# Performance work log

Measured on AMD Instinct MI355X. Metric: run time of the kernel, lower is better.

## Reference

```python
import jax, jax.numpy as jnp
import numpy as np

B, T, C, H, N = 2, 1024, 2048, 32, 64
KVH = 8                       # GQA kv heads
KV = KVH * N                  # 512
REP = H // KVH                # 4
EPS = 1e-6
LORA = [96, 96, 64, 256, 64]  # xw, xa, xv, xg, xk lora dims


def rmsnorm(x, w, eps=EPS):
    xf = x.astype(jnp.float32)
    var = jnp.mean(xf * xf, axis=-1, keepdims=True)
    return (w * (xf * jax.lax.rsqrt(var + eps))).astype(x.dtype)


def rotate_half(x):
    x1, x2 = jnp.split(x, 2, axis=-1)
    return jnp.concatenate([-x2, x1], axis=-1)


def rwkv7_scan(r, w, k, v, a, b, state0):
    # r,w,k,v,a,b: [B,T,H,N]; state0: [B,H,N,N] (value x key)
    # per step: S = S*exp(w) + (S@a) b^T + v k^T ; o = S @ r
    def step(S, inp):
        r_t, w_t, k_t, v_t, a_t, b_t = inp  # each [B,H,N]
        sa = jnp.einsum('bhvk,bhk->bhv', S, a_t)
        S = (S * jnp.exp(w_t)[:, :, None, :]
             + sa[..., None] * b_t[:, :, None, :]
             + v_t[..., None] * k_t[:, :, None, :])
        o = jnp.einsum('bhvk,bhk->bhv', S, r_t)
        return S, o
    seqs = tuple(jnp.moveaxis(t, 1, 0) for t in (r, w, k, v, a, b))
    S, o = jax.lax.scan(step, state0, seqs)
    return jnp.moveaxis(o, 0, 1), S


def setup_inputs() -> dict:
    key = jax.random.key(0)
    ks = jax.random.split(key, 24)
    g = lambda i, shape, s=0.02: jax.random.normal(ks[i], shape, jnp.float32) * s
    # real rope cache, theta = 1e6, rotary_dim = N
    pos = jnp.arange(T, dtype=jnp.float32)
    inv = 1.0 / (1e6 ** (jnp.arange(0, N, 2, dtype=jnp.float32) / N))
    ang = pos[:, None] * inv[None, :]
    ang = jnp.concatenate([ang, ang], axis=-1)  # [T, N]
    cos = jnp.broadcast_to(jnp.cos(ang)[None], (B, T, N))
    sin = jnp.broadcast_to(jnp.sin(ang)[None], (B, T, N))
    return dict(
        x_in=jax.random.normal(ks[0], (B, T, C), jnp.float32),
        v_first=jax.random.normal(ks[1], (B, T, KVH, N), jnp.float32),
        k_first=jax.random.normal(ks[2], (B, T, KVH, N), jnp.float32),
        state=jnp.zeros((B, H, N, N), jnp.float32),
        calc_cos=cos, calc_sin=sin,
        ln1=jnp.ones((C,), jnp.float32), ln2=jnp.ones((C,), jnp.float32),
        ln_r=jnp.ones((N,), jnp.float32), ln_k=jnp.ones((N,), jnp.float32),
        wavgk1=g(3, (C, sum(LORA))),
        w0=g(4, (H * N,)), w2=g(5, (LORA[0], H * N)),
        a0=g(6, (H * N,)), a2=g(7, (LORA[1], H * N)),
        v0=g(8, (KV,)), v2=g(9, (LORA[2], KV)),
        k0=g(10, (KV,)), k2=g(11, (LORA[4], KV)),
        g2=g(12, (LORA[3], H * N)),
        r_k=g(13, (H, N)),
        RKV_W=g(14, (C, H * N + 2 * KV)),
        O_W=g(15, (H * N, C)),
        R_bias=g(16, (H * N,)), K_bias=g(17, (KV,)), V_bias=g(18, (KV,)),
    )


def _forward(x_in, v_first, k_first, state, calc_cos, calc_sin,
             ln1, ln2, ln_r, ln_k, wavgk1, w0, w2, a0, a2, v0, v2,
             k0, k2, g2, r_k, RKV_W, O_W, R_bias, K_bias, V_bias):
    x = rmsnorm(x_in, ln1)
    xw, xa, xv, xg, xk = jnp.split(x @ wavgk1, np.cumsum(LORA)[:-1].tolist(), axis=-1)
    r, k, v = jnp.split(x @ RKV_W, [H * N, H * N + KV], axis=-1)
    r = (r + R_bias).reshape(B, T, H, N)
    k = (k + K_bias).reshape(B, T, KVH, N)
    v = (v + V_bias).reshape(B, T, KVH, N)
    r = rmsnorm(r, ln_r)
    k = rmsnorm(k, ln_k)
    cos = calc_cos[:, :, None, :]
    sin = calc_sin[:, :, None, :]
    r = r * cos + rotate_half(r) * sin
    k = k * cos + rotate_half(k) * sin
    # layer_id != 0: sigmoid-gated interpolation toward first-layer v/k
    v = v + (v_first - v) * jax.nn.sigmoid(xv @ v2 + v0).reshape(B, T, KVH, N)
    k = k + (k_first - k) * jax.nn.sigmoid(xk @ k2 + k0).reshape(B, T, KVH, N)
    # GQA repeat (contiguous per kv head, as repeat_kv does)
    k = jnp.repeat(k, REP, axis=2).reshape(B, T, H * N)
    v = jnp.repeat(v, REP, axis=2).reshape(B, T, H * N)
    a = jax.nn.sigmoid(xa @ a2 + a0)
    kh = k.reshape(B, T, H, N)
    kk = (kh / (jnp.linalg.norm(kh, axis=-1, keepdims=True) + 1e-12)).reshape(B, T, H * N)
    w = jnp.tanh(xw) @ w2 + w0
    w = -jax.nn.softplus(-w) - 0.5
    k = k * (1.0 - w + a)
    aa = -kk
    bb = kk * a
    wlog = -jnp.exp(w)
    sh = (B, T, H, N)
    o, state = rwkv7_scan(r, wlog.reshape(sh), k.reshape(sh), v.reshape(sh),
                          aa.reshape(sh), bb.reshape(sh), state)
    xx = o.reshape(B, T, H * N) * (float(N) ** -0.5)
    bonus = ((r * k.reshape(sh) * r_k).sum(axis=-1, keepdims=True)
             * v.reshape(sh)).reshape(B, T, H * N)
    xx = xx + bonus
    out = (xx * (jax.nn.sigmoid(xg) @ g2)) @ O_W
    x_res = x_in + out
    output = rmsnorm(x_res, ln2)
    return output, x[:, -1], state, v_first, k_first, x_res


def reference(x_in, v_first, k_first, state, calc_cos, calc_sin,
              ln1, ln2, ln_r, ln_k, wavgk1, w0, w2, a0, a2, v0, v2,
              k0, k2, g2, r_k, RKV_W, O_W, R_bias, K_bias, V_bias):
    return _forward(x_in, v_first, k_first, state, calc_cos, calc_sin,
                    ln1, ln2, ln_r, ln_k, wavgk1, w0, w2, a0, a2, v0, v2,
                    k0, k2, g2, r_k, RKV_W, O_W, R_bias, K_bias, V_bias)
```

## Files before the change

kernel.cpp:

```cpp
#include <hip/hip_runtime.h>
#include <hip/hip_bf16.h>

#define BT 2
#define TT 1024
#define CC 2048
#define HH 32
#define MM (BT*TT)
#define TCH 512
#define NCH (TT/TCH)
#define RECB 896

typedef __attribute__((ext_vector_type(8))) short short8;
typedef __attribute__((ext_vector_type(4))) float floatx4;
typedef __attribute__((ext_vector_type(2))) float f32x2;

static __device__ __forceinline__ float bf2f(__hip_bfloat16 x){ return __bfloat162float(x); }
static __device__ __forceinline__ __hip_bfloat16 f2bf(float x){ return __float2bfloat16(x); }
static __device__ __forceinline__ float sigm(float x){ return 1.0f/(1.0f + expf(-x)); }
static __device__ __forceinline__ float u2f(unsigned short u){
  union { unsigned int i; float f; } x; x.i = ((unsigned int)u) << 16; return x.f;
}
static __device__ __forceinline__ float ulo(unsigned int u){ return __uint_as_float(u << 16); }
static __device__ __forceinline__ float uhi(unsigned int u){ return __uint_as_float(u & 0xffff0000u); }
static __device__ __forceinline__ unsigned short bfbits(float x){
  __hip_bfloat16 h = f2bf(x);
  unsigned short s; __builtin_memcpy(&s, &h, 2); return s;
}
static __device__ __forceinline__ unsigned int pkbf(float lo, float hi){
  return (unsigned int)bfbits(lo) | ((unsigned int)bfbits(hi) << 16);
}

#if defined(__has_builtin)
#if __has_builtin(__builtin_amdgcn_global_load_lds)
#define HAVE_GLL 1
#endif
#endif

#ifdef HAVE_GLL
static __device__ __forceinline__ void gll16(const void* g, void* l){
  __builtin_amdgcn_global_load_lds(
      (__attribute__((address_space(1))) void*)const_cast<void*>(g),
      (__attribute__((address_space(3))) void*)l,
      16, 0, 0);
}
#endif

#define DPP_ADD(x, ctrl) ((x) + __int_as_float(__builtin_amdgcn_update_dpp(0, __float_as_int(x), (ctrl), 0xF, 0xF, true)))

#if defined(__has_builtin)
#if __has_builtin(__builtin_amdgcn_permlane16_swap) && __has_builtin(__builtin_amdgcn_permlane32_swap)
#define HAVE_PLSWAP 1
#endif
#endif

#ifdef HAVE_PLSWAP
typedef unsigned int uint2v __attribute__((ext_vector_type(2)));
static __device__ __forceinline__ float row16_pair_add(float x){
  unsigned int u = __float_as_uint(x);
  uint2v r = __builtin_amdgcn_permlane16_swap(u, u, false, false);
  return __uint_as_float(r[0]) + __uint_as_float(r[1]);
}
static __device__ __forceinline__ float half32_pair_add(float x){
  unsigned int u = __float_as_uint(x);
  uint2v r = __builtin_amdgcn_permlane32_swap(u, u, false, false);
  return __uint_as_float(r[0]) + __uint_as_float(r[1]);
}
#else
static __device__ __forceinline__ float row16_pair_add(float x){ return x + __shfl_xor(x, 16); }
static __device__ __forceinline__ float half32_pair_add(float x){ return x + __shfl_xor(x, 32); }
#endif

static __device__ __forceinline__ float red8(float x){
  x = DPP_ADD(x, 0xB1);
  x = DPP_ADD(x, 0x4E);
  x = DPP_ADD(x, 0x141);
  return x;
}
static __device__ __forceinline__ float red32(float x){
  x = DPP_ADD(x, 0xB1);
  x = DPP_ADD(x, 0x4E);
  x = DPP_ADD(x, 0x124);
  x = DPP_ADD(x, 0x128);
  return row16_pair_add(x);
}
static __device__ __forceinline__ float red64(float x){
  x = DPP_ADD(x, 0xB1);
  x = DPP_ADD(x, 0x4E);
  x = DPP_ADD(x, 0x124);
  x = DPP_ADD(x, 0x128);
  x = row16_pair_add(x);
  return half32_pair_add(x);
}

__global__ __launch_bounds__(256) void tcvt_kernel(
    const float* __restrict__ W, __hip_bfloat16* __restrict__ Wt,
    int K, int N, int Npad)
{
  __shared__ float tile[32][33];
  const int bn = blockIdx.x*32, bk = blockIdx.y*32;
  const int tx = threadIdx.x & 31, ty0 = threadIdx.x >> 5;
#pragma unroll
  for (int i=0;i<4;++i){
    const int kk = bk + ty0 + i*8;
    float val = 0.f;
    if (kk < K && bn + tx < N) val = W[(size_t)kk*N + bn + tx];
    tile[ty0 + i*8][tx] = val;
  }
  __syncthreads();
#pragma unroll
  for (int i=0;i<4;++i){
    const int nn = bn + ty0 + i*8;
    const int kk = bk + tx;
    if (nn < Npad && kk < K) Wt[(size_t)nn*K + kk] = f2bf(tile[tx][ty0 + i*8]);
  }
}

__global__ __launch_bounds__(256) void rmsnorm1_kernel(
    const float* __restrict__ x_in,
    const float* __restrict__ ln1,
    __hip_bfloat16* __restrict__ x_bf,
    float* __restrict__ x_last)
{
  const int m = blockIdx.x;
  const int tid = threadIdx.x;
  const int c = tid * 8;
  const float* xp = x_in + (size_t)m*CC + c;
  float v[8]; float ss = 0.f;
#pragma unroll
  for (int i=0;i<8;++i){ v[i] = xp[i]; ss += v[i]*v[i]; }
  ss = red64(ss);
  __shared__ float wsum[4];
  if ((tid&63)==0) wsum[tid>>6] = ss;
  __syncthreads();
  ss = wsum[0]+wsum[1]+wsum[2]+wsum[3];
  const float sc = rsqrtf(ss * (1.0f/CC) + 1e-6f);
#pragma unroll
  for (int i=0;i<8;++i) {
    const float y = ln1[c+i] * v[i] * sc;
    x_bf[(size_t)m*CC + c + i] = f2bf(y);
    if ((m % TT) == TT-1) x_last[(size_t)(m/TT)*CC + c + i] = y;
  }
}

template<bool F32OUT, int ACT>
__global__ __launch_bounds__(256) void mgemm(
    const __hip_bfloat16* __restrict__ A, int lda,
    const __hip_bfloat16* __restrict__ Bt,
    void* __restrict__ C, int N, int K)
{
  __shared__ __align__(16) short As[128*32];
  __shared__ __align__(16) short Bs[128*32];
  const int tid = threadIdx.x;
  const int bm = blockIdx.x * 128;
  const int bn = blockIdx.y * 128;
  const int wid = tid >> 6;
  const int lane = tid & 63;
  const int m16 = lane & 15, quad = lane >> 4;
  const int wm = wid & 1, wn = wid >> 1;
  const int lrow = tid >> 2;
  const int lcol = (tid & 3) * 8;

  floatx4 acc[4][4];
#pragma unroll
  for (int i=0;i<4;++i)
#pragma unroll
    for (int j=0;j<4;++j) acc[i][j] = (floatx4){0.f,0.f,0.f,0.f};

  char* asl = (char*)As + tid*16;
  char* bsl = (char*)Bs + tid*16;

  for (int k0 = 0; k0 < K; k0 += 32) {
    __syncthreads();
#ifdef HAVE_GLL
    gll16(A  + (size_t)(bm + lrow)      * lda + k0 + lcol, asl);
    gll16(A  + (size_t)(bm + 64 + lrow) * lda + k0 + lcol, asl + 4096);
    gll16(Bt + (size_t)(bn + lrow)      * K   + k0 + lcol, bsl);
    gll16(Bt + (size_t)(bn + 64 + lrow) * K   + k0 + lcol, bsl + 4096);
#else
    uint4 a0v = *(const uint4*)(const void*)(A  + (size_t)(bm + lrow)      * lda + k0 + lcol);
    uint4 a1v = *(const uint4*)(const void*)(A  + (size_t)(bm + 64 + lrow) * lda + k0 + lcol);
    uint4 b0v = *(const uint4*)(const void*)(Bt + (size_t)(bn + lrow)      * K   + k0 + lcol);
    uint4 b1v = *(const uint4*)(const void*)(Bt + (size_t)(bn + 64 + lrow) * K   + k0 + lcol);
    *(uint4*)(void*)(asl)        = a0v;
    *(uint4*)(void*)(asl + 4096) = a1v;
    *(uint4*)(void*)(bsl)        = b0v;
    *(uint4*)(void*)(bsl + 4096) = b1v;
#endif
    __syncthreads();

    short8 af[4], bfg[4];
#pragma unroll
    for (int mi=0; mi<4; ++mi)
      af[mi] = *(const short8*)(const void*)(As + (wm*64 + mi*16 + m16)*32 + quad*8);
#pragma unroll
    for (int ni=0; ni<4; ++ni)
      bfg[ni] = *(const short8*)(const void*)(Bs + (wn*64 + ni*16 + m16)*32 + quad*8);
#pragma unroll
    for (int mi=0; mi<4; ++mi)
#pragma unroll
      for (int ni=0; ni<4; ++ni)
        acc[mi][ni] = __builtin_amdgcn_mfma_f32_16x16x32_bf16(af[mi], bfg[ni], acc[mi][ni], 0,0,0);
  }

#pragma unroll
  for (int mi=0; mi<4; ++mi) {
    const int row = bm + wm*64 + mi*16 + quad*4;
#pragma unroll
    for (int ni=0; ni<4; ++ni) {
      const int col = bn + wn*64 + ni*16 + m16;
      if (col < N) {
        if (F32OUT) {
          float* cp = (float*)C;
#pragma unroll
          for (int r=0;r<4;++r) cp[(size_t)(row+r)*N + col] = acc[mi][ni][r];
        } else {
          __hip_bfloat16* cp = (__hip_bfloat16*)C;
#pragma unroll
          for (int r=0;r<4;++r) {
            float x = acc[mi][ni][r];
            if (ACT == 1) {
              if (col < 96) x = tanhf(x);
              else if (col >= 256 && col < 512) x = sigm(x);
            }
            cp[(size_t)(row+r)*N + col] = f2bf(x);
          }
        }
      }
    }
  }
}

__global__ __launch_bounds__(256) void prep_kernel(
    const __hip_bfloat16* __restrict__ RKV,
    const __hip_bfloat16* __restrict__ Wpre,
    const __hip_bfloat16* __restrict__ Apre,
    const __hip_bfloat16* __restrict__ Vsig,
    const __hip_bfloat16* __restrict__ Ksig,
    const float* __restrict__ v_first,
    const float* __restrict__ k_first,
    const float* __restrict__ cosp,
    const float* __restrict__ sinp,
    const float* __restrict__ ln_r,
    const float* __restrict__ ln_k,
    const float* __restrict__ r_k,
    const float* __restrict__ w0,
    const float* __restrict__ a0,
    const float* __restrict__ v0,
    const float* __restrict__ k0b,
    const float* __restrict__ R_bias,
    const float* __restrict__ K_bias,
    const float* __restrict__ V_bias,
    char* __restrict__ rec,
    float* __restrict__ bonus,
    int t0)
{
  const int b    = blockIdx.x / TCH;
  const int tloc = blockIdx.x % TCH;
  const int t    = t0 + tloc;
  const int m    = b*TT + t;
  const int tid = threadIdx.x;
  const int h  = tid >> 3;
  const int j  = tid & 7;
  const int hk = h >> 2;
  const int nb = j * 8;
  const int hn = h*64 + nb;
  const int kn = hk*64 + nb;

  const size_t rbase = (size_t)m*3072 + h*64 + nb;
  const size_t kbase = (size_t)m*3072 + 2048 + kn;
  const size_t vbase = kbase + 512;

  float r[8], k[8], v[8];
  float ssr = 0.f, ssk = 0.f;
#pragma unroll
  for (int i=0;i<8;++i) {
    r[i] = bf2f(RKV[rbase+i]) + R_bias[hn+i];
    k[i] = bf2f(RKV[kbase+i]) + K_bias[kn+i];
    v[i] = bf2f(RKV[vbase+i]) + V_bias[kn+i];
    ssr += r[i]*r[i];
    ssk += k[i]*k[i];
  }
  ssr = red8(ssr);
  ssk = red8(ssk);
  const float scr = rsqrtf(ssr*(1.0f/64.0f) + 1e-6f);
  const float sck = rsqrtf(ssk*(1.0f/64.0f) + 1e-6f);
#pragma unroll
  for (int i=0;i<8;++i) {
    r[i] = ln_r[nb+i] * r[i] * scr;
    k[i] = ln_k[nb+i] * k[i] * sck;
  }
  const float sgn = (j < 4) ? -1.0f : 1.0f;
  float rr[8], kr[8];
#pragma unroll
  for (int i=0;i<8;++i) {
    const float cs = cosp[(size_t)m*64 + nb + i];
    const float sn = sinp[(size_t)m*64 + nb + i];
    const float pr = __shfl_xor(r[i], 4);
    const float pk = __shfl_xor(k[i], 4);
    rr[i] = r[i]*cs + sgn*pr*sn;
    kr[i] = k[i]*cs + sgn*pk*sn;
  }
  float av[8], ew[8], wv2[8];
  float ssn = 0.f;
#pragma unroll
  for (int i=0;i<8;++i) {
    const float vs = sigm(bf2f(Vsig[(size_t)m*512 + kn + i]) + v0[kn+i]);
    v[i]  = v[i]  + (v_first[(size_t)m*512 + kn + i] - v[i])  * vs;
    const float ks = sigm(bf2f(Ksig[(size_t)m*512 + kn + i]) + k0b[kn+i]);
    kr[i] = kr[i] + (k_first[(size_t)m*512 + kn + i] - kr[i]) * ks;
    ssn += kr[i]*kr[i];
    av[i] = sigm(bf2f(Apre[(size_t)m*2048 + hn + i]) + a0[hn+i]);
    float wraw = bf2f(Wpre[(size_t)m*2048 + hn + i]) + w0[hn+i];
    const float xs = -wraw;
    const float sp = fmaxf(xs, 0.f) + log1pf(expf(-fabsf(xs)));
    const float wv = -sp - 0.5f;
    wv2[i] = wv;
    ew[i] = expf(-expf(wv));
  }
  ssn = red8(ssn);
  const float inrm = 1.0f / (sqrtf(ssn) + 1e-12f);
  float kf[8], kkv[8];
  float bsum = 0.f;
#pragma unroll
  for (int i=0;i<8;++i) {
    kkv[i] = kr[i] * inrm;
    kf[i]  = kr[i] * (1.0f - wv2[i] + av[i]);
    bsum  += rr[i] * kf[i] * r_k[hn+i];
  }
  bsum = red8(bsum);

  char* base = rec + ((size_t)(b*HH + h)*TCH + tloc)*RECB;
  const int klb = nb >> 1;
#pragma unroll
  for (int p=0;p<4;++p) {
    const int i0 = 2*p, i1 = i0 + 1;
    uint4 Aw;
    Aw.x = __float_as_uint(ew[i0]);
    Aw.y = __float_as_uint(ew[i1]);
    Aw.z = pkbf(rr[i0], rr[i1]);
    Aw.w = pkbf(kf[i0], kf[i1]);
    *(uint4*)(void*)(base + (size_t)(klb + p)*16) = Aw;
    uint2 Bw;
    Bw.x = pkbf(kkv[i0], kkv[i1]);
    Bw.y = pkbf(-kkv[i0]*av[i0], -kkv[i1]*av[i1]);
    *(uint2*)(void*)(base + 512 + (size_t)(klb + p)*8) = Bw;
  }
  short8 vs8;
#pragma unroll
  for (int i=0;i<8;++i) vs8[i] = (short)bfbits(v[i]);
  *(short8*)(void*)(base + 768 + (size_t)nb*2) = vs8;
#pragma unroll
  for (int i=0;i<8;++i)
    bonus[(size_t)m*2048 + hn + i] = bsum * v[i];
}

__global__ __launch_bounds__(256) void scan_kernel(
    const char* __restrict__ rec,
    float* __restrict__ state,
    float* __restrict__ o_out,
    int t0)
{
  const int blk = blockIdx.x;
  const int bh  = blk & 63;
  const int q   = blk >> 6;
  const int b   = bh >> 5, h = bh & 31;
  const int tid = threadIdx.x;
  const int vl  = q*8 + (tid >> 5);
  const int kl  = tid & 31;
  const int k2  = kl*2;

  const char* base = rec + (size_t)bh * TCH * RECB;
  float* sp = state + ((size_t)bh*64 + vl)*64 + k2;
  f32x2 S; S.x = sp[0]; S.y = sp[1];

  const char* pA = base + kl*16;
  const char* pB = base + 512 + kl*8;
  const char* pv = base + 768 + vl*2;

  uint4 Ab[4]; uint2 Bb[4]; unsigned short vb[4];
#pragma unroll
  for (int s=0;s<4;++s){
    Ab[s] = *(const uint4*)(const void*)(pA + s*RECB);
    Bb[s] = *(const uint2*)(const void*)(pB + s*RECB);
    vb[s] = *(const unsigned short*)(const void*)(pv + s*RECB);
  }
  pA += 4*RECB; pB += 4*RECB; pv += 4*RECB;

  int oidx = (b*TT + t0)*CC + h*64 + vl - CC;
  float opart = 0.f;

#define SCAN_STEP(jj, PF, ST)                                                  \
  {                                                                            \
    const uint4 A  = Ab[jj];                                                   \
    const uint2 Bv = Bb[jj];                                                   \
    const float vf = u2f(vb[jj]);                                              \
    if (PF) {                                                                  \
      Ab[jj] = *(const uint4*)(const void*)(pA + jj*RECB);                     \
      Bb[jj] = *(const uint2*)(const void*)(pB + jj*RECB);                     \
      vb[jj] = *(const unsigned short*)(const void*)(pv + jj*RECB);            \
    }                                                                          \
    float op = red32(opart);                                                   \
    f32x2 kk; kk.x = ulo(Bv.x); kk.y = uhi(Bv.x);                              \
    const f32x2 prod = S * kk;                                                 \
    float sa = prod.x + prod.y;                                                \
    sa = red32(sa);                                                            \
    if (ST && kl == 0) o_out[oidx] = op;                                       \
    f32x2 ew; ew.x = __uint_as_float(A.x); ew.y = __uint_as_float(A.y);        \
    f32x2 bb; bb.x = ulo(Bv.y); bb.y = uhi(Bv.y);                              \
    f32x2 kf; kf.x = ulo(A.w); kf.y = uhi(A.w);                                \
    f32x2 sav; sav.x = sa; sav.y = sa;                                         \
    f32x2 vfv; vfv.x = vf; vfv.y = vf;                                         \
    S = S*ew + sav*bb + vfv*kf;                                                \
    f32x2 rv; rv.x = ulo(A.z); rv.y = uhi(A.z);                                \
    const f32x2 ov = S * rv;                                                   \
    opart = ov.x + ov.y;                                                       \
    oidx += CC;                                                                \
  }

  SCAN_STEP(0, true, 0)
  SCAN_STEP(1, true, 1)
  SCAN_STEP(2, true, 1)
  SCAN_STEP(3, true, 1)
  pA += 4*RECB; pB += 4*RECB; pv += 4*RECB;

  for (int t = 4; t < TCH-4; t += 4) {
    SCAN_STEP(0, true, 1)
    SCAN_STEP(1, true, 1)
    SCAN_STEP(2, true, 1)
    SCAN_STEP(3, true, 1)
    pA += 4*RECB; pB += 4*RECB; pv += 4*RECB;
  }
  SCAN_STEP(0, false, 1)
  SCAN_STEP(1, false, 1)
  SCAN_STEP(2, false, 1)
  SCAN_STEP(3, false, 1)
#undef SCAN_STEP

  opart = red32(opart);
  if (kl == 0)
    o_out[oidx] = opart;

  sp[0]=S.x; sp[1]=S.y;
}

__global__ void xxg_kernel(const float* __restrict__ o_in,
                           const float* __restrict__ bonus,
                           const __hip_bfloat16* __restrict__ G,
                           __hip_bfloat16* __restrict__ xxg)
{
  int i = blockIdx.x*256 + threadIdx.x;
  xxg[i] = f2bf((o_in[i]*0.125f + bonus[i]) * bf2f(G[i]));
}

__global__ __launch_bounds__(256) void final_kernel(
    const float* __restrict__ x_in,
    const float* __restrict__ OUTb,
    const float* __restrict__ ln2,
    float* __restrict__ seg0,
    float* __restrict__ seg5)
{
  const int m = blockIdx.x;
  const int tid = threadIdx.x;
  const int c = tid*8;
  const float* xp = x_in + (size_t)m*CC + c;
  const float* op = OUTb + (size_t)m*CC + c;
  float xr[8]; float ss = 0.f;
#pragma unroll
  for (int i=0;i<8;++i){ xr[i] = xp[i] + op[i]; ss += xr[i]*xr[i]; }
#pragma unroll
  for (int i=0;i<8;++i) seg5[(size_t)m*CC + c + i] = xr[i];
  ss = red64(ss);
  __shared__ float wsum[4];
  if ((tid&63)==0) wsum[tid>>6] = ss;
  __syncthreads();
  ss = wsum[0]+wsum[1]+wsum[2]+wsum[3];
  const float sc = rsqrtf(ss*(1.0f/CC) + 1e-6f);
#pragma unroll
  for (int i=0;i<8;++i) seg0[(size_t)m*CC + c + i] = ln2[c+i] * xr[i] * sc;
}

extern "C" void kernel_launch(void* const* d_in, const int* in_sizes, int n_in,
                              void* d_out, int out_size, void* d_ws, size_t ws_size,
                              hipStream_t stream)
{
  (void)in_sizes; (void)n_in; (void)out_size; (void)ws_size;
  const float* x_in   = (const float*)d_in[0];
  const float* v_first= (const float*)d_in[1];
  const float* k_first= (const float*)d_in[2];
  const float* state0 = (const float*)d_in[3];
  const float* cosp   = (const float*)d_in[4];
  const float* sinp   = (const float*)d_in[5];
  const float* ln1    = (const float*)d_in[6];
  const float* ln2    = (const float*)d_in[7];
  const float* ln_r   = (const float*)d_in[8];
  const float* ln_k   = (const float*)d_in[9];
  const float* wavgk1 = (const float*)d_in[10];
  const float* w0     = (const float*)d_in[11];
  const float* w2     = (const float*)d_in[12];
  const float* a0     = (const float*)d_in[13];
  const float* a2     = (const float*)d_in[14];
  const float* v0     = (const float*)d_in[15];
  const float* v2     = (const float*)d_in[16];
  const float* k0b    = (const float*)d_in[17];
  const float* k2     = (const float*)d_in[18];
  const float* g2     = (const float*)d_in[19];
  const float* r_k    = (const float*)d_in[20];
  const float* RKV_W  = (const float*)d_in[21];
  const float* O_W    = (const float*)d_in[22];
  const float* R_bias = (const float*)d_in[23];
  const float* K_bias = (const float*)d_in[24];
  const float* V_bias = (const float*)d_in[25];

  float* out  = (float*)d_out;
  float* seg0 = out;
  float* seg1 = out + 4194304;
  float* seg2 = out + 4198400;
  float* seg3 = out + 4460544;
  float* seg4 = out + 5509120;
  float* seg5 = out + 6557696;

  char* ws = (char*)d_ws;
  const size_t OFF_STF   = 0;
  const size_t OFF_OWT   = 1048576;
  const size_t OFF_G     = 9437184;
  const size_t OFF_VSIG  = 17825792;
  const size_t OFF_KSIG  = 19922944;
  const size_t OFF_WPRE  = 22020096;
  const size_t OFF_APRE  = 30408704;
  const size_t OFF_RKV   = 38797312;
  const size_t OFF_XBF   = 51380224;
  const size_t OFF_Y1    = 59768832;
  const size_t OFF_WT    = 62128128;
  const size_t OFF_WAVT  = OFF_WT;
  const size_t OFF_RKVT  = OFF_WAVT + 2621440;
  const size_t OFF_W2T   = OFF_RKVT + 12582912;
  const size_t OFF_A2T   = OFF_W2T  + 393216;
  const size_t OFF_V2T   = OFF_A2T  + 393216;
  const size_t OFF_K2T   = OFF_V2T  + 65536;
  const size_t OFF_G2T   = OFF_K2T  + 65536;
  const size_t OFF_REC   = OFF_WT;
  const size_t OFF_XXG   = OFF_XBF;
  const size_t OFF_OUT   = OFF_WPRE;

  float*          stf   = (float*)(ws + OFF_STF);
  __hip_bfloat16* owt   = (__hip_bfloat16*)(ws + OFF_OWT);
  __hip_bfloat16* Gbuf  = (__hip_bfloat16*)(ws + OFF_G);
  __hip_bfloat16* Vsig  = (__hip_bfloat16*)(ws + OFF_VSIG);
  __hip_bfloat16* Ksig  = (__hip_bfloat16*)(ws + OFF_KSIG);
  __hip_bfloat16* Wpre  = (__hip_bfloat16*)(ws + OFF_WPRE);
  __hip_bfloat16* Apre  = (__hip_bfloat16*)(ws + OFF_APRE);
  __hip_bfloat16* RKV   = (__hip_bfloat16*)(ws + OFF_RKV);
  __hip_bfloat16* x_bf  = (__hip_bfloat16*)(ws + OFF_XBF);
  __hip_bfloat16* Y1    = (__hip_bfloat16*)(ws + OFF_Y1);
  __hip_bfloat16* wavt  = (__hip_bfloat16*)(ws + OFF_WAVT);
  __hip_bfloat16* rkvt  = (__hip_bfloat16*)(ws + OFF_RKVT);
  __hip_bfloat16* w2t   = (__hip_bfloat16*)(ws + OFF_W2T);
  __hip_bfloat16* a2t   = (__hip_bfloat16*)(ws + OFF_A2T);
  __hip_bfloat16* v2t   = (__hip_bfloat16*)(ws + OFF_V2T);
  __hip_bfloat16* k2t   = (__hip_bfloat16*)(ws + OFF_K2T);
  __hip_bfloat16* g2t   = (__hip_bfloat16*)(ws + OFF_G2T);
  char*           rec   = ws + OFF_REC;
  __hip_bfloat16* xxg   = (__hip_bfloat16*)(ws + OFF_XXG);
  float*          OUTb  = (float*)(ws + OFF_OUT);

  float* o_st = seg0;
  float* b_st = seg5;

  tcvt_kernel<<<dim3(20, 64), 256, 0, stream>>>(wavgk1, wavt, 2048, 576, 640);
  tcvt_kernel<<<dim3(96, 64), 256, 0, stream>>>(RKV_W,  rkvt, 2048, 3072, 3072);
  tcvt_kernel<<<dim3(64, 64), 256, 0, stream>>>(O_W,    owt,  2048, 2048, 2048);
  tcvt_kernel<<<dim3(64,  3), 256, 0, stream>>>(w2,     w2t,    96, 2048, 2048);
  tcvt_kernel<<<dim3(64,  3), 256, 0, stream>>>(a2,     a2t,    96, 2048, 2048);
  tcvt_kernel<<<dim3(16,  2), 256, 0, stream>>>(v2,     v2t,    64,  512,  512);
  tcvt_kernel<<<dim3(16,  2), 256, 0, stream>>>(k2,     k2t,    64,  512,  512);
  tcvt_kernel<<<dim3(64,  8), 256, 0, stream>>>(g2,     g2t,   256, 2048, 2048);

  rmsnorm1_kernel<<<MM, 256, 0, stream>>>(x_in, ln1, x_bf, seg1);
  mgemm<false,1><<<dim3(16,  5), 256, 0, stream>>>(x_bf, CC, wavt, Y1,   576, 2048);
  mgemm<false,0><<<dim3(16, 24), 256, 0, stream>>>(x_bf, CC, rkvt, RKV, 3072, 2048);
  mgemm<false,0><<<dim3(16, 16), 256, 0, stream>>>(Y1+0,   576, w2t, Wpre, 2048, 96);
  mgemm<false,0><<<dim3(16, 16), 256, 0, stream>>>(Y1+96,  576, a2t, Apre, 2048, 96);
  mgemm<false,0><<<dim3(16,  4), 256, 0, stream>>>(Y1+192, 576, v2t, Vsig,  512, 64);
  mgemm<false,0><<<dim3(16,  4), 256, 0, stream>>>(Y1+512, 576, k2t, Ksig,  512, 64);
  mgemm<false,0><<<dim3(16, 16), 256, 0, stream>>>(Y1+256, 576, g2t, Gbuf, 2048, 256);

  hipMemcpyAsync(stf, state0, (size_t)1048576, hipMemcpyDeviceToDevice, stream);
  for (int c = 0; c < NCH; ++c) {
    const int t0 = c*TCH;
    prep_kernel<<<BT*TCH, 256, 0, stream>>>(RKV, Wpre, Apre, Vsig, Ksig, v_first, k_first,
                                            cosp, sinp, ln_r, ln_k, r_k, w0, a0, v0, k0b,
                                            R_bias, K_bias, V_bias, rec, b_st, t0);
    scan_kernel<<<BT*HH*8, 256, 0, stream>>>(rec, stf, o_st, t0);
  }
  hipMemcpyAsync(seg2, stf, (size_t)1048576, hipMemcpyDeviceToDevice, stream);

  xxg_kernel<<<(MM*CC)/256, 256, 0, stream>>>(o_st, b_st, Gbuf, xxg);
  mgemm<true,0><<<dim3(16, 16), 256, 0, stream>>>(xxg, CC, owt, OUTb, 2048, 2048);
  final_kernel<<<MM, 256, 0, stream>>>(x_in, OUTb, ln2, seg0, seg5);

  hipMemcpyAsync(seg3, v_first, (size_t)1048576*4, hipMemcpyDeviceToDevice, stream);
  hipMemcpyAsync(seg4, k_first, (size_t)1048576*4, hipMemcpyDeviceToDevice, stream);
}
```

Baseline: 664.8 us.

## Merge LoRA up-projections into one block-diagonal GEMM and pair scan steps

```diff
diff --git a/kernel.cpp b/kernel.cpp
--- a/kernel.cpp
+++ b/kernel.cpp
@@ -8,11 +8,11 @@
 #define MM (BT*TT)
 #define TCH 512
 #define NCH (TT/TCH)
+#define YS 7168
 #define RECB 896
 
 typedef __attribute__((ext_vector_type(8))) short short8;
 typedef __attribute__((ext_vector_type(4))) float floatx4;
-typedef __attribute__((ext_vector_type(2))) float f32x2;
 
 static __device__ __forceinline__ float bf2f(__hip_bfloat16 x){ return __bfloat162float(x); }
 static __device__ __forceinline__ __hip_bfloat16 f2bf(float x){ return __float2bfloat16(x); }
@@ -94,7 +94,7 @@
 
 __global__ __launch_bounds__(256) void tcvt_kernel(
     const float* __restrict__ W, __hip_bfloat16* __restrict__ Wt,
-    int K, int N, int Npad)
+    int K, int N, int Npad, int wstride)
 {
   __shared__ float tile[32][33];
   const int bn = blockIdx.x*32, bk = blockIdx.y*32;
@@ -111,8 +111,13 @@
   for (int i=0;i<4;++i){
     const int nn = bn + ty0 + i*8;
     const int kk = bk + tx;
-    if (nn < Npad && kk < K) Wt[(size_t)nn*K + kk] = f2bf(tile[tx][ty0 + i*8]);
-  }
+    if (nn < Npad && kk < K) Wt[(size_t)nn*wstride + kk] = f2bf(tile[tx][ty0 + i*8]);
+  }
+}
+
+__global__ void zfill_kernel(uint4* __restrict__ p)
+{
+  p[(size_t)blockIdx.x*256 + threadIdx.x] = (uint4){0,0,0,0};
 }
 
 __global__ __launch_bounds__(256) void rmsnorm1_kernel(
@@ -232,10 +237,7 @@
 
 __global__ __launch_bounds__(256) void prep_kernel(
     const __hip_bfloat16* __restrict__ RKV,
-    const __hip_bfloat16* __restrict__ Wpre,
-    const __hip_bfloat16* __restrict__ Apre,
-    const __hip_bfloat16* __restrict__ Vsig,
-    const __hip_bfloat16* __restrict__ Ksig,
+    const __hip_bfloat16* __restrict__ Yb,
     const float* __restrict__ v_first,
     const float* __restrict__ k_first,
     const float* __restrict__ cosp,
@@ -269,6 +271,7 @@
   const size_t rbase = (size_t)m*3072 + h*64 + nb;
   const size_t kbase = (size_t)m*3072 + 2048 + kn;
   const size_t vbase = kbase + 512;
+  const size_t ybase = (size_t)m*YS;
 
   float r[8], k[8], v[8];
   float ssr = 0.f, ssk = 0.f;
@@ -304,13 +307,13 @@
   float ssn = 0.f;
 #pragma unroll
   for (int i=0;i<8;++i) {
-    const float vs = sigm(bf2f(Vsig[(size_t)m*512 + kn + i]) + v0[kn+i]);
+    const float vs = sigm(bf2f(Yb[ybase + 4096 + kn + i]) + v0[kn+i]);
     v[i]  = v[i]  + (v_first[(size_t)m*512 + kn + i] - v[i])  * vs;
-    const float ks = sigm(bf2f(Ksig[(size_t)m*512 + kn + i]) + k0b[kn+i]);
+    const float ks = sigm(bf2f(Yb[ybase + 4608 + kn + i]) + k0b[kn+i]);
     kr[i] = kr[i] + (k_first[(size_t)m*512 + kn + i] - kr[i]) * ks;
     ssn += kr[i]*kr[i];
-    av[i] = sigm(bf2f(Apre[(size_t)m*2048 + hn + i]) + a0[hn+i]);
-    float wraw = bf2f(Wpre[(size_t)m*2048 + hn + i]) + w0[hn+i];
+    av[i] = sigm(bf2f(Yb[ybase + 2048 + hn + i]) + a0[hn+i]);
+    float wraw = bf2f(Yb[ybase + hn + i]) + w0[hn+i];
     const float xs = -wraw;
     const float sp = fmaxf(xs, 0.f) + log1pf(expf(-fabsf(xs)));
     const float wv = -sp - 0.5f;
@@ -371,85 +374,99 @@
 
   const char* base = rec + (size_t)bh * TCH * RECB;
   float* sp = state + ((size_t)bh*64 + vl)*64 + k2;
-  f32x2 S; S.x = sp[0]; S.y = sp[1];
+  float S0=sp[0], S1=sp[1];
 
   const char* pA = base + kl*16;
   const char* pB = base + 512 + kl*8;
   const char* pv = base + 768 + vl*2;
 
-  uint4 Ab[4]; uint2 Bb[4]; unsigned short vb[4];
-#pragma unroll
-  for (int s=0;s<4;++s){
-    Ab[s] = *(const uint4*)(const void*)(pA + s*RECB);
-    Bb[s] = *(const uint2*)(const void*)(pB + s*RECB);
-    vb[s] = *(const unsigned short*)(const void*)(pv + s*RECB);
-  }
+  uint4 A1x, A2x, A1y, A2y;
+  uint2 B1x, B2x, B1y, B2y;
+  unsigned short v1x, v2x, v1y, v2y;
+
+  A1x = *(const uint4*)(const void*)(pA);
+  B1x = *(const uint2*)(const void*)(pB);
+  v1x = *(const unsigned short*)(const void*)(pv);
+  A2x = *(const uint4*)(const void*)(pA + RECB);
+  B2x = *(const uint2*)(const void*)(pB + RECB);
+  v2x = *(const unsigned short*)(const void*)(pv + RECB);
+  A1y = *(const uint4*)(const void*)(pA + 2*RECB);
+  B1y = *(const uint2*)(const void*)(pB + 2*RECB);
+  v1y = *(const unsigned short*)(const void*)(pv + 2*RECB);
+  A2y = *(const uint4*)(const void*)(pA + 3*RECB);
+  B2y = *(const uint2*)(const void*)(pB + 3*RECB);
+  v2y = *(const unsigned short*)(const void*)(pv + 3*RECB);
   pA += 4*RECB; pB += 4*RECB; pv += 4*RECB;
 
-  int oidx = (b*TT + t0)*CC + h*64 + vl - CC;
-  float opart = 0.f;
-
-#define SCAN_STEP(jj, PF, ST)                                                  \
+  int oidx = (b*TT + t0)*CC + h*64 + vl - 2*CC;
+  float o1d = 0.f, o2d = 0.f;
+
+#define PAIR(A1,B1,v1,A2,B2,v2, PF, PFOFF, ST)                                 \
   {                                                                            \
-    const uint4 A  = Ab[jj];                                                   \
-    const uint2 Bv = Bb[jj];                                                   \
-    const float vf = u2f(vb[jj]);                                              \
+              \
+    const float oa = red32(o1d);                                               \
+    const float ob = red32(o2d);                                               \
+    if (ST && kl == 0) { o_out[oidx] = oa; o_out[oidx + CC] = ob; }            \
+    oidx += 2*CC;                                                              \
+                                              \
+    const float kk20 = ulo(B2.x), kk21 = uhi(B2.x);                            \
+    const float c1 = red32(ulo(B1.y)*kk20 + uhi(B1.y)*kk21);                   \
+    const float c2 = red32(ulo(A1.w)*kk20 + uhi(A1.w)*kk21);                   \
+                             \
+    const float kk10 = ulo(B1.x), kk11 = uhi(B1.x);                            \
+    const float ew10 = __uint_as_float(A1.x), ew11 = __uint_as_float(A1.y);    \
+    const float d1 = red32(S0*kk10 + S1*kk11);                                 \
+    const float d2 = red32(S0*(ew10*kk20) + S1*(ew11*kk21));                   \
+    const float vf1 = u2f(v1), vf2 = u2f(v2);                                  \
+    const float sa1 = d1;                                                      \
+    S0 = S0*ew10 + sa1*ulo(B1.y) + vf1*ulo(A1.w);                              \
+    S1 = S1*ew11 + sa1*uhi(B1.y) + vf1*uhi(A1.w);                              \
+    o1d = S0*ulo(A1.z) + S1*uhi(A1.z);                                         \
+    const float sa2 = d2 + sa1*c1 + vf1*c2;                                    \
+    S0 = S0*__uint_as_float(A2.x) + sa2*ulo(B2.y) + vf2*ulo(A2.w);             \
+    S1 = S1*__uint_as_float(A2.y) + sa2*uhi(B2.y) + vf2*uhi(A2.w);             \
+    o2d = S0*ulo(A2.z) + S1*uhi(A2.z);                                         \
     if (PF) {                                                                  \
-      Ab[jj] = *(const uint4*)(const void*)(pA + jj*RECB);                     \
-      Bb[jj] = *(const uint2*)(const void*)(pB + jj*RECB);                     \
-      vb[jj] = *(const unsigned short*)(const void*)(pv + jj*RECB);            \
+      A1 = *(const uint4*)(const void*)(pA + (PFOFF));                         \
+      B1 = *(const uint2*)(const void*)(pB + (PFOFF));                         \
+      v1 = *(const unsigned short*)(const void*)(pv + (PFOFF));                \
+      A2 = *(const uint4*)(const void*)(pA + (PFOFF) + RECB);                  \
+      B2 = *(const uint2*)(const void*)(pB + (PFOFF) + RECB);                  \
+      v2 = *(const unsigned short*)(const void*)(pv + (PFOFF) + RECB);         \
     }                                                                          \
-    float op = red32(opart);                                                   \
-    f32x2 kk; kk.x = ulo(Bv.x); kk.y = uhi(Bv.x);                              \
-    const f32x2 prod = S * kk;                                                 \
-    float sa = prod.x + prod.y;                                                \
-    sa = red32(sa);                                                            \
-    if (ST && kl == 0) o_out[oidx] = op;                                       \
-    f32x2 ew; ew.x = __uint_as_float(A.x); ew.y = __uint_as_float(A.y);        \
-    f32x2 bb; bb.x = ulo(Bv.y); bb.y = uhi(Bv.y);                              \
-    f32x2 kf; kf.x = ulo(A.w); kf.y = uhi(A.w);                                \
-    f32x2 sav; sav.x = sa; sav.y = sa;                                         \
-    f32x2 vfv; vfv.x = vf; vfv.y = vf;                                         \
-    S = S*ew + sav*bb + vfv*kf;                                                \
-    f32x2 rv; rv.x = ulo(A.z); rv.y = uhi(A.z);                                \
-    const f32x2 ov = S * rv;                                                   \
-    opart = ov.x + ov.y;                                                       \
-    oidx += CC;                                                                \
-  }
-
-  SCAN_STEP(0, true, 0)
-  SCAN_STEP(1, true, 1)
-  SCAN_STEP(2, true, 1)
-  SCAN_STEP(3, true, 1)
+  }
+
+  PAIR(A1x,B1x,v1x,A2x,B2x,v2x, 1, 0,        0)
+  PAIR(A1y,B1y,v1y,A2y,B2y,v2y, 1, 2*RECB,   1)
   pA += 4*RECB; pB += 4*RECB; pv += 4*RECB;
 
-  for (int t = 4; t < TCH-4; t += 4) {
-    SCAN_STEP(0, true, 1)
-    SCAN_STEP(1, true, 1)
-    SCAN_STEP(2, true, 1)
-    SCAN_STEP(3, true, 1)
+  for (int p = 2; p < TCH/2 - 2; p += 2) {
+    PAIR(A1x,B1x,v1x,A2x,B2x,v2x, 1, 0,      1)
+    PAIR(A1y,B1y,v1y,A2y,B2y,v2y, 1, 2*RECB, 1)
     pA += 4*RECB; pB += 4*RECB; pv += 4*RECB;
   }
-  SCAN_STEP(0, false, 1)
-  SCAN_STEP(1, false, 1)
-  SCAN_STEP(2, false, 1)
-  SCAN_STEP(3, false, 1)
-#undef SCAN_STEP
-
-  opart = red32(opart);
-  if (kl == 0)
-    o_out[oidx] = opart;
-
-  sp[0]=S.x; sp[1]=S.y;
+  PAIR(A1x,B1x,v1x,A2x,B2x,v2x, 0, 0, 1)
+  PAIR(A1y,B1y,v1y,A2y,B2y,v2y, 0, 0, 1)
+#undef PAIR
+
+  {
+    const float oa = red32(o1d);
+    const float ob = red32(o2d);
+    if (kl == 0) { o_out[oidx] = oa; o_out[oidx + CC] = ob; }
+  }
+
+  sp[0]=S0; sp[1]=S1;
 }
 
 __global__ void xxg_kernel(const float* __restrict__ o_in,
                            const float* __restrict__ bonus,
-                           const __hip_bfloat16* __restrict__ G,
+                           const __hip_bfloat16* __restrict__ Yb,
                            __hip_bfloat16* __restrict__ xxg)
 {
   int i = blockIdx.x*256 + threadIdx.x;
-  xxg[i] = f2bf((o_in[i]*0.125f + bonus[i]) * bf2f(G[i]));
+  const int m = i >> 11, c = i & 2047;
+  const float g = bf2f(Yb[(size_t)m*YS + 5120 + c]);
+  xxg[i] = f2bf((o_in[i]*0.125f + bonus[i]) * g);
 }
 
 __global__ __launch_bounds__(256) void final_kernel(
@@ -522,43 +539,27 @@
   char* ws = (char*)d_ws;
   const size_t OFF_STF   = 0;
   const size_t OFF_OWT   = 1048576;
-  const size_t OFF_G     = 9437184;
-  const size_t OFF_VSIG  = 17825792;
-  const size_t OFF_KSIG  = 19922944;
-  const size_t OFF_WPRE  = 22020096;
-  const size_t OFF_APRE  = 30408704;
+  const size_t OFF_YB    = 9437184;
   const size_t OFF_RKV   = 38797312;
   const size_t OFF_XBF   = 51380224;
   const size_t OFF_Y1    = 59768832;
   const size_t OFF_WT    = 62128128;
   const size_t OFF_WAVT  = OFF_WT;
   const size_t OFF_RKVT  = OFF_WAVT + 2621440;
-  const size_t OFF_W2T   = OFF_RKVT + 12582912;
-  const size_t OFF_A2T   = OFF_W2T  + 393216;
-  const size_t OFF_V2T   = OFF_A2T  + 393216;
-  const size_t OFF_K2T   = OFF_V2T  + 65536;
-  const size_t OFF_G2T   = OFF_K2T  + 65536;
+  const size_t OFF_WM    = OFF_RKVT + 12582912;
   const size_t OFF_REC   = OFF_WT;
   const size_t OFF_XXG   = OFF_XBF;
-  const size_t OFF_OUT   = OFF_WPRE;
+  const size_t OFF_OUT   = OFF_YB;
 
   float*          stf   = (float*)(ws + OFF_STF);
   __hip_bfloat16* owt   = (__hip_bfloat16*)(ws + OFF_OWT);
-  __hip_bfloat16* Gbuf  = (__hip_bfloat16*)(ws + OFF_G);
-  __hip_bfloat16* Vsig  = (__hip_bfloat16*)(ws + OFF_VSIG);
-  __hip_bfloat16* Ksig  = (__hip_bfloat16*)(ws + OFF_KSIG);
-  __hip_bfloat16* Wpre  = (__hip_bfloat16*)(ws + OFF_WPRE);
-  __hip_bfloat16* Apre  = (__hip_bfloat16*)(ws + OFF_APRE);
+  __hip_bfloat16* Yb    = (__hip_bfloat16*)(ws + OFF_YB);
   __hip_bfloat16* RKV   = (__hip_bfloat16*)(ws + OFF_RKV);
   __hip_bfloat16* x_bf  = (__hip_bfloat16*)(ws + OFF_XBF);
   __hip_bfloat16* Y1    = (__hip_bfloat16*)(ws + OFF_Y1);
   __hip_bfloat16* wavt  = (__hip_bfloat16*)(ws + OFF_WAVT);
   __hip_bfloat16* rkvt  = (__hip_bfloat16*)(ws + OFF_RKVT);
-  __hip_bfloat16* w2t   = (__hip_bfloat16*)(ws + OFF_W2T);
-  __hip_bfloat16* a2t   = (__hip_bfloat16*)(ws + OFF_A2T);
-  __hip_bfloat16* v2t   = (__hip_bfloat16*)(ws + OFF_V2T);
-  __hip_bfloat16* k2t   = (__hip_bfloat16*)(ws + OFF_K2T);
-  __hip_bfloat16* g2t   = (__hip_bfloat16*)(ws + OFF_G2T);
+  __hip_bfloat16* Wm    = (__hip_bfloat16*)(ws + OFF_WM);
   char*           rec   = ws + OFF_REC;
   __hip_bfloat16* xxg   = (__hip_bfloat16*)(ws + OFF_XXG);
   float*          OUTb  = (float*)(ws + OFF_OUT);
@@ -566,35 +567,32 @@
   float* o_st = seg0;
   float* b_st = seg5;
 
-  tcvt_kernel<<<dim3(20, 64), 256, 0, stream>>>(wavgk1, wavt, 2048, 576, 640);
-  tcvt_kernel<<<dim3(96, 64), 256, 0, stream>>>(RKV_W,  rkvt, 2048, 3072, 3072);
-  tcvt_kernel<<<dim3(64, 64), 256, 0, stream>>>(O_W,    owt,  2048, 2048, 2048);
-  tcvt_kernel<<<dim3(64,  3), 256, 0, stream>>>(w2,     w2t,    96, 2048, 2048);
-  tcvt_kernel<<<dim3(64,  3), 256, 0, stream>>>(a2,     a2t,    96, 2048, 2048);
-  tcvt_kernel<<<dim3(16,  2), 256, 0, stream>>>(v2,     v2t,    64,  512,  512);
-  tcvt_kernel<<<dim3(16,  2), 256, 0, stream>>>(k2,     k2t,    64,  512,  512);
-  tcvt_kernel<<<dim3(64,  8), 256, 0, stream>>>(g2,     g2t,   256, 2048, 2048);
+  tcvt_kernel<<<dim3(20, 64), 256, 0, stream>>>(wavgk1, wavt, 2048, 576, 640, 2048);
+  tcvt_kernel<<<dim3(96, 64), 256, 0, stream>>>(RKV_W,  rkvt, 2048, 3072, 3072, 2048);
+  tcvt_kernel<<<dim3(64, 64), 256, 0, stream>>>(O_W,    owt,  2048, 2048, 2048, 2048);
+  zfill_kernel<<<2016, 256, 0, stream>>>((uint4*)(void*)Wm);
+  tcvt_kernel<<<dim3(64,  3), 256, 0, stream>>>(w2, Wm + (size_t)0*576    + 0,   96, 2048, 2048, 576);
+  tcvt_kernel<<<dim3(64,  3), 256, 0, stream>>>(a2, Wm + (size_t)2048*576 + 96,  96, 2048, 2048, 576);
+  tcvt_kernel<<<dim3(16,  2), 256, 0, stream>>>(v2, Wm + (size_t)4096*576 + 192, 64,  512,  512, 576);
+  tcvt_kernel<<<dim3(16,  2), 256, 0, stream>>>(k2, Wm + (size_t)4608*576 + 512, 64,  512,  512, 576);
+  tcvt_kernel<<<dim3(64,  8), 256, 0, stream>>>(g2, Wm + (size_t)5120*576 + 256, 256, 2048, 2048, 576);
 
   rmsnorm1_kernel<<<MM, 256, 0, stream>>>(x_in, ln1, x_bf, seg1);
   mgemm<false,1><<<dim3(16,  5), 256, 0, stream>>>(x_bf, CC, wavt, Y1,   576, 2048);
   mgemm<false,0><<<dim3(16, 24), 256, 0, stream>>>(x_bf, CC, rkvt, RKV, 3072, 2048);
-  mgemm<false,0><<<dim3(16, 16), 256, 0, stream>>>(Y1+0,   576, w2t, Wpre, 2048, 96);
-  mgemm<false,0><<<dim3(16, 16), 256, 0, stream>>>(Y1+96,  576, a2t, Apre, 2048, 96);
-  mgemm<false,0><<<dim3(16,  4), 256, 0, stream>>>(Y1+192, 576, v2t, Vsig,  512, 64);
-  mgemm<false,0><<<dim3(16,  4), 256, 0, stream>>>(Y1+512, 576, k2t, Ksig,  512, 64);
-  mgemm<false,0><<<dim3(16, 16), 256, 0, stream>>>(Y1+256, 576, g2t, Gbuf, 2048, 256);
+  mgemm<false,0><<<dim3(16, 56), 256, 0, stream>>>(Y1,   576, Wm,   Yb,  7168,  576);
 
   hipMemcpyAsync(stf, state0, (size_t)1048576, hipMemcpyDeviceToDevice, stream);
   for (int c = 0; c < NCH; ++c) {
     const int t0 = c*TCH;
-    prep_kernel<<<BT*TCH, 256, 0, stream>>>(RKV, Wpre, Apre, Vsig, Ksig, v_first, k_first,
+    prep_kernel<<<BT*TCH, 256, 0, stream>>>(RKV, Yb, v_first, k_first,
                                             cosp, sinp, ln_r, ln_k, r_k, w0, a0, v0, k0b,
                                             R_bias, K_bias, V_bias, rec, b_st, t0);
     scan_kernel<<<BT*HH*8, 256, 0, stream>>>(rec, stf, o_st, t0);
   }
   hipMemcpyAsync(seg2, stf, (size_t)1048576, hipMemcpyDeviceToDevice, stream);
 
-  xxg_kernel<<<(MM*CC)/256, 256, 0, stream>>>(o_st, b_st, Gbuf, xxg);
+  xxg_kernel<<<(MM*CC)/256, 256, 0, stream>>>(o_st, b_st, Yb, xxg);
   mgemm<true,0><<<dim3(16, 16), 256, 0, stream>>>(xxg, CC, owt, OUTb, 2048, 2048);
   final_kernel<<<MM, 256, 0, stream>>>(x_in, OUTb, ln2, seg0, seg5);
 
```

New measurement: 698.3 us. 1.05x slower.
